# Optimization experiments

Measured on AMD Instinct MI355X. Metric: run time of the kernel, lower is better.

## Reference

```python
import jax, jax.numpy as jnp
import numpy as np

B, N, P = 16, 128, 4096          # images, proposals/img, pairs/img
D_IN, D_HID = 1024, 512          # input_dim, hidden_dim
D_GEO, D_EMB = 128, 200          # geometry_feat_dim, embed_dim
N_OBJ, N_REL = 151, 51           # obj classes, rel classes (out_dim = 50)
OUT = N_REL - 1
LN_EPS = 1e-5


def _ln(x, g, b):
    mu = jnp.mean(x, axis=-1, keepdims=True)
    var = jnp.var(x, axis=-1, keepdims=True)
    return (x - mu) * jax.lax.rsqrt(var + LN_EPS) * g + b


def setup_inputs() -> dict:
    key = jax.random.key(0)
    ks = jax.random.split(key, 20)
    w = lambda k, shape: (jax.random.normal(k, shape, jnp.float32) * 0.02)
    return {
        'visual_feat': jax.random.normal(ks[0], (B * P, D_IN), jnp.float32),
        'box_info': jax.random.uniform(ks[1], (B, N, 9), jnp.float32),
        'pred_logits': jax.random.normal(ks[2], (B, N, N_OBJ), jnp.float32),
        'pair_idx': jax.random.randint(ks[3], (B, P, 2), 0, N, jnp.int32),
        'obj_sem_w': w(ks[4], (N_OBJ, D_EMB)),
        'pos_w1': w(ks[5], (9, D_GEO)), 'pos_b1': jnp.zeros((D_GEO,), jnp.float32),
        'pos_w2': w(ks[6], (D_GEO, D_GEO)), 'pos_b2': jnp.zeros((D_GEO,), jnp.float32),
        'vis_w': w(ks[7], (D_IN, D_HID)), 'vis_b': jnp.zeros((D_HID,), jnp.float32),
        'geo_w': w(ks[8], (2 * D_EMB + 2 * D_GEO, D_HID)), 'geo_b': jnp.zeros((D_HID,), jnp.float32),
        'fus_g': jnp.ones((2 * D_HID,), jnp.float32), 'fus_bt': jnp.zeros((2 * D_HID,), jnp.float32),
        'fus_w': w(ks[9], (2 * D_HID, D_HID)), 'fus_b': jnp.zeros((D_HID,), jnp.float32),
        'cls_g': jnp.ones((D_HID,), jnp.float32), 'cls_bt': jnp.zeros((D_HID,), jnp.float32),
        'cls_w': w(ks[10], (D_HID, OUT)), 'cls_b': jnp.zeros((OUT,), jnp.float32),
    }


def reference(visual_feat, box_info, pred_logits, pair_idx,
              obj_sem_w, pos_w1, pos_b1, pos_w2, pos_b2,
              vis_w, vis_b, geo_w, geo_b,
              fus_g, fus_bt, fus_w, fus_b,
              cls_g, cls_bt, cls_w, cls_b):
    # detach() in torch -> stop_gradient
    vf = jax.lax.stop_gradient(visual_feat)
    pl = jax.lax.stop_gradient(pred_logits)
    # vis_embed = Sequential(ReLU, Linear): [B*P, D_IN] -> [B, P, D_HID]
    vis = (jnp.maximum(vf, 0.0) @ vis_w + vis_b).reshape(B, P, D_HID)
    # obj_pos_embed = Linear, ReLU, Linear: [B, N, 9] -> [B, N, D_GEO]
    pos = jnp.maximum(box_info @ pos_w1 + pos_b1, 0.0) @ pos_w2 + pos_b2
    # semantic embed: softmax over obj classes @ embedding table -> [B, N, D_EMB]
    sem = jax.nn.softmax(pl, axis=-1) @ obj_sem_w
    bidx = jnp.arange(B)[:, None]
    s, o = pair_idx[..., 0], pair_idx[..., 1]
    # gather pair reps: [B, P, 2*(D_GEO+D_EMB)]
    rep = jnp.concatenate([pos[bidx, s], sem[bidx, s], pos[bidx, o], sem[bidx, o]], axis=-1)
    # proposal_box_feat_extract = Sequential(ReLU, Linear)
    geo = jnp.maximum(rep, 0.0) @ geo_w + geo_b
    # proposal_feat_fusion = Sequential(LayerNorm, ReLU, Linear)
    fused = jnp.concatenate([vis, geo], axis=-1)
    fused = jnp.maximum(_ln(fused, fus_g, fus_bt), 0.0) @ fus_w + fus_b
    # proposal_relness_cls_fc = Sequential(LayerNorm, ReLU, Linear)
    logits = jnp.maximum(_ln(fused, cls_g, cls_bt), 0.0) @ cls_w + cls_b  # [B, P, OUT]
    # predictor_type == 'single': scatter max sigmoid score into NxN matrix
    scores = jnp.max(jax.nn.sigmoid(logits), axis=-1)  # [B, P]
    rel_mat = jnp.zeros((B, N, N), logits.dtype).at[bidx, s, o].set(scores)
    return logits.reshape(B * P, OUT), rel_mat
```

## Files before the change

kernel.cpp:

```cpp
#include <hip/hip_runtime.h>
#include <cstdint>

#define B_    16
#define N_    128
#define P_    4096
#define M_    65536
#define DIN   1024
#define DHID  512
#define DGEO  128
#define DEMB  200
#define NODEF 328
#define NOBJ  151
#define OUTC  50
#define KGEO  656
#define KGEOP 672

typedef __attribute__((ext_vector_type(8))) short bf16x8;
typedef __attribute__((ext_vector_type(4))) float f32x4;

typedef __attribute__((address_space(3))) unsigned char lds_u8;
typedef __attribute__((address_space(1))) unsigned char glb_u8;

static __device__ __forceinline__ void async_copy16(const void* g, void* l) {
  __builtin_amdgcn_global_load_lds((const glb_u8*)g, (lds_u8*)l, 16, 0, 0);
}

static __device__ __forceinline__ unsigned short f2b(float f) {
  union { float f; unsigned u; } v; v.f = f;
  unsigned r = v.u + 0x7fffu + ((v.u >> 16) & 1u);
  return (unsigned short)(r >> 16);
}
static __device__ __forceinline__ float b2f(unsigned short b) {
  union { unsigned u; float f; } v; v.u = ((unsigned)b) << 16;
  return v.f;
}
static __device__ __forceinline__ unsigned pack2(float a, float b) {
  return (unsigned)f2b(a) | ((unsigned)f2b(b) << 16);
}
static __device__ __forceinline__ void unpack8(uint4 raw, float* x) {
  x[0] = b2f(raw.x & 0xffffu); x[1] = b2f(raw.x >> 16);
  x[2] = b2f(raw.y & 0xffffu); x[3] = b2f(raw.y >> 16);
  x[4] = b2f(raw.z & 0xffffu); x[5] = b2f(raw.z >> 16);
  x[6] = b2f(raw.w & 0xffffu); x[7] = b2f(raw.w >> 16);
}

#define ZN   131072
#define TV   (512 * 1024)
#define TG   (512 * KGEOP)
#define TF   (512 * 1024)
#define TC   (128 * 512)
#define PREP_TOT (ZN + TV + TG + TF + TC)
__global__ __launch_bounds__(256)
void prep_kernel(uint4* __restrict__ scat,
                 const float* __restrict__ vis_w, unsigned short* __restrict__ wT_vis,
                 const float* __restrict__ geo_w, unsigned short* __restrict__ wT_geo,
                 const float* __restrict__ fus_w, unsigned short* __restrict__ wT_fus,
                 const float* __restrict__ cls_w, unsigned short* __restrict__ wT_cls) {
  int idx = blockIdx.x * 256 + threadIdx.x;
  if (idx < ZN) { scat[idx] = make_uint4(0, 0, 0, 0); return; }
  idx -= ZN;
  if (idx < TV) {
    int n = idx >> 10, k = idx & 1023;
    wT_vis[idx] = f2b(vis_w[(size_t)k * 512 + n]);
    return;
  }
  idx -= TV;
  if (idx < TG) {
    int n = idx / KGEOP, k = idx - n * KGEOP;
    wT_geo[idx] = (k < KGEO) ? f2b(geo_w[(size_t)k * 512 + n]) : 0;
    return;
  }
  idx -= TG;
  if (idx < TF) {
    int n = idx >> 10, k = idx & 1023;
    wT_fus[idx] = f2b(fus_w[(size_t)k * 512 + n]);
    return;
  }
  idx -= TF;
  if (idx < TC) {
    int n = idx >> 9, k = idx & 511;
    wT_cls[idx] = (n < OUTC) ? f2b(cls_w[(size_t)k * OUTC + n]) : 0;
  }
}

__global__ __launch_bounds__(128)
void node_kernel(const float* __restrict__ box, const float* __restrict__ plog,
                 const float* __restrict__ semw,
                 const float* __restrict__ w1, const float* __restrict__ b1,
                 const float* __restrict__ w2, const float* __restrict__ b2,
                 unsigned short* __restrict__ nodeFb) {
  const int node = blockIdx.x;
  const int t = threadIdx.x;
  __shared__ float sBox[9];
  __shared__ float sH[128];
  __shared__ float sE[NOBJ];
  __shared__ float sRed[4];
  if (t < 9) sBox[t] = box[node * 9 + t];
  float l0 = (t < NOBJ) ? plog[node * NOBJ + t] : -1e30f;
  float l1 = (t + 128 < NOBJ) ? plog[node * NOBJ + t + 128] : -1e30f;
  __syncthreads();
  float h = b1[t];
#pragma unroll
  for (int i = 0; i < 9; i++) h = fmaf(sBox[i], w1[i * 128 + t], h);
  h = fmaxf(h, 0.f);
  sH[t] = h;
  float mx = fmaxf(l0, l1);
#pragma unroll
  for (int off = 32; off >= 1; off >>= 1) mx = fmaxf(mx, __shfl_xor(mx, off));
  if ((t & 63) == 0) sRed[t >> 6] = mx;
  __syncthreads();
  mx = fmaxf(sRed[0], sRed[1]);
  float e0 = (t < NOBJ) ? expf(l0 - mx) : 0.f;
  float e1 = (t + 128 < NOBJ) ? expf(l1 - mx) : 0.f;
  if (t < NOBJ) sE[t] = e0;
  if (t + 128 < NOBJ) sE[t + 128] = e1;
  float sm = e0 + e1;
#pragma unroll
  for (int off = 32; off >= 1; off >>= 1) sm += __shfl_xor(sm, off);
  if ((t & 63) == 0) sRed[2 + (t >> 6)] = sm;
  __syncthreads();
  const float inv = 1.f / (sRed[2] + sRed[3]);
  float pv = b2[t];
  for (int i = 0; i < 128; i++) pv = fmaf(sH[i], w2[i * 128 + t], pv);
  nodeFb[(size_t)node * NODEF + t] = f2b(fmaxf(pv, 0.f));
  float a0 = 0.f, a1 = 0.f;
  const int d1 = (t + 128 < DEMB) ? (t + 128) : 0;
  for (int i = 0; i < NOBJ; i++) {
    float e = sE[i];
    a0 = fmaf(e, semw[i * DEMB + t], a0);
    a1 = fmaf(e, semw[i * DEMB + d1], a1);
  }
  nodeFb[(size_t)node * NODEF + 128 + t] = f2b(fmaxf(a0 * inv, 0.f));
  if (t + 128 < DEMB) nodeFb[(size_t)node * NODEF + 128 + t + 128] = f2b(fmaxf(a1 * inv, 0.f));
}

template<int D>
__global__ __launch_bounds__(256)
void ln_relu_kernel(unsigned short* __restrict__ X,
                    const float* __restrict__ g, const float* __restrict__ bta) {
  constexpr int C = D / 64;
  const int lane = threadIdx.x & 63, wv = threadIdx.x >> 6;
  const size_t row = (size_t)blockIdx.x * 4 + wv;
  unsigned short* xp = X + row * D + lane * C;
  float x[C];
#pragma unroll
  for (int c = 0; c < C; c += 8) {
    uint4 raw = *(const uint4*)(xp + c);
    unpack8(raw, x + c);
  }
  float s = 0.f, s2 = 0.f;
#pragma unroll
  for (int q = 0; q < C; q++) { s += x[q]; s2 = fmaf(x[q], x[q], s2); }
#pragma unroll
  for (int off = 32; off >= 1; off >>= 1) { s += __shfl_xor(s, off); s2 += __shfl_xor(s2, off); }
  const float mu = s / D;
  const float rs = rsqrtf(s2 / D - mu * mu + 1e-5f);
  const float* gp = g + lane * C;
  const float* bp = bta + lane * C;
#pragma unroll
  for (int c = 0; c < C; c += 8) {
    float4 g0 = *(const float4*)(gp + c), g1 = *(const float4*)(gp + c + 4);
    float4 t0 = *(const float4*)(bp + c), t1 = *(const float4*)(bp + c + 4);
    float y0 = fmaxf(fmaf((x[c + 0] - mu) * rs, g0.x, t0.x), 0.f);
    float y1 = fmaxf(fmaf((x[c + 1] - mu) * rs, g0.y, t0.y), 0.f);
    float y2 = fmaxf(fmaf((x[c + 2] - mu) * rs, g0.z, t0.z), 0.f);
    float y3 = fmaxf(fmaf((x[c + 3] - mu) * rs, g0.w, t0.w), 0.f);
    float y4 = fmaxf(fmaf((x[c + 4] - mu) * rs, g1.x, t1.x), 0.f);
    float y5 = fmaxf(fmaf((x[c + 5] - mu) * rs, g1.y, t1.y), 0.f);
    float y6 = fmaxf(fmaf((x[c + 6] - mu) * rs, g1.z, t1.z), 0.f);
    float y7 = fmaxf(fmaf((x[c + 7] - mu) * rs, g1.w, t1.w), 0.f);
    uint4 u;
    u.x = pack2(y0, y1); u.y = pack2(y2, y3);
    u.z = pack2(y4, y5); u.w = pack2(y6, y7);
    *(uint4*)(xp + c) = u;
  }
}

static __device__ __forceinline__ int pair_swz(int bid, int nwg) {
  const int cpx2 = nwg >> 4;
  const int pr = bid >> 1, q = bid & 1;
  return (((pr & 7) * cpx2) + (pr >> 3)) * 2 + q;
}

template<int MODE>
__global__ __launch_bounds__(512)
void gemm256r(const unsigned short* __restrict__ A, int ldaE,
              const unsigned short* __restrict__ Bt, int ldbE,
              const float* __restrict__ bias,
              unsigned short* __restrict__ C, int ldcE, int ccol0,
              int NS, int NBN,
              const int* __restrict__ pidx,
              const unsigned short* __restrict__ nodeFb,
              const unsigned short* __restrict__ zsrc) {
  __shared__ __align__(16) unsigned char smem[131072];
  const int tid = threadIdx.x;
  const int lane = tid & 63, w = tid >> 6;
  const int swz = pair_swz(blockIdx.x, gridDim.x);
  const int bm = swz / NBN, bn = swz - bm * NBN;

  const int sslot = (tid & 3) ^ ((tid >> 3) & 3);
  const int srow = tid >> 2;
  const size_t ldaBy = (size_t)ldaE * 2, ldbBy = (size_t)ldbE * 2;
  const unsigned char* aG = (const unsigned char*)A + (size_t)(bm * 256 + srow) * ldaBy + sslot * 16;
  const unsigned char* bG = (const unsigned char*)Bt + (size_t)(bn * 256 + srow) * ldbBy + sslot * 16;

  const unsigned short* nbS[2];
  const unsigned short* nbO[2];
  if (MODE == 1) {
#pragma unroll
    for (int r = 0; r < 2; r++) {
      int pr = bm * 256 + r * 128 + srow;
      int2 so = *(const int2*)(pidx + 2 * pr);
      int b = pr >> 12;
      nbS[r] = nodeFb + (size_t)((b << 7) + so.x) * NODEF;
      nbO[r] = nodeFb + (size_t)((b << 7) + so.y) * NODEF;
    }
  }

  auto stage = [&](int s) {
    const int slot = s & 3;
    unsigned char* la = smem + slot * 16384 + w * 1024;
    unsigned char* lb = smem + 65536 + slot * 16384 + w * 1024;
    if (MODE == 0) {
      const unsigned char* sa = aG + (size_t)s * 64;
      async_copy16(sa, la);
      async_copy16(sa + 128 * ldaBy, la + 8192);
    } else {
      const int e = s * 32 + sslot * 8;
#pragma unroll
      for (int r = 0; r < 2; r++) {
        uintptr_t ps = (uintptr_t)(nbS[r] + e);
        uintptr_t po = (uintptr_t)(nbO[r] + (e - NODEF));
        uintptr_t pz = (uintptr_t)zsrc;
        uintptr_t sel = (e < NODEF) ? ps : ((e < KGEO) ? po : pz);
        async_copy16((const void*)sel, la + r * 8192);
      }
    }
    const unsigned char* sb = bG + (size_t)s * 64;
    async_copy16(sb, lb);
    async_copy16(sb + 128 * ldbBy, lb + 8192);
  };

  const int wm = w >> 2, wn = w & 3;
  const int frow = lane & 15;
  const int colb = (((lane >> 4) ^ ((frow >> 1) & 3)) << 4);
  const int aRowB = (wm * 128 + frow) * 64;
  const int bRowB = (wn * 64 + frow) * 64;

  f32x4 acc[8][4];
#pragma unroll
  for (int m = 0; m < 8; m++)
#pragma unroll
    for (int n = 0; n < 4; n++) acc[m][n] = (f32x4){0.f, 0.f, 0.f, 0.f};

  stage(0); stage(1); stage(2);
  for (int s = 0; s < NS; ++s) {
    if (s == NS - 1)      asm volatile("s_waitcnt vmcnt(0)" ::: "memory");
    else if (s == NS - 2) asm volatile("s_waitcnt vmcnt(4)" ::: "memory");
    else                  asm volatile("s_waitcnt vmcnt(8)" ::: "memory");
    __builtin_amdgcn_s_barrier();
    __builtin_amdgcn_sched_barrier(0);
    if (s + 3 < NS) stage(s + 3);
    const unsigned char* ab = smem + (s & 3) * 16384;
    const unsigned char* bb = smem + 65536 + (s & 3) * 16384;
    bf16x8 af[8], bfv[4];
#pragma unroll
    for (int m = 0; m < 8; m++) af[m] = *(const bf16x8*)(ab + aRowB + m * 1024 + colb);
#pragma unroll
    for (int n = 0; n < 4; n++) bfv[n] = *(const bf16x8*)(bb + bRowB + n * 1024 + colb);
    __builtin_amdgcn_s_setprio(1);
#pragma unroll
    for (int m = 0; m < 8; m++)
#pragma unroll
      for (int n = 0; n < 4; n++)
        acc[m][n] = __builtin_amdgcn_mfma_f32_16x16x32_bf16(af[m], bfv[n], acc[m][n], 0, 0, 0);
    __builtin_amdgcn_s_setprio(0);
    __builtin_amdgcn_sched_barrier(0);
  }
  const int rb = bm * 256 + wm * 128 + ((lane >> 4) << 2);
  const int cb = bn * 256 + wn * 64 + frow;
#pragma unroll
  for (int n = 0; n < 4; n++) {
    const int col = cb + n * 16;
    const float bv = bias[col];
#pragma unroll
    for (int m = 0; m < 8; m++)
#pragma unroll
      for (int i = 0; i < 4; i++) {
        const int row = rb + m * 16 + i;
        C[(size_t)row * ldcE + ccol0 + col] = f2b(acc[m][n][i] + bv);
      }
  }
}

__global__ __launch_bounds__(512)
void gemm256f(const float* __restrict__ A,
              const unsigned short* __restrict__ Bt,
              const float* __restrict__ bias,
              unsigned short* __restrict__ C, int ldcE, int ccol0,
              int NBN) {
  constexpr int NS = 32;
  __shared__ __align__(16) unsigned char smem[131072];
  const int tid = threadIdx.x;
  const int lane = tid & 63, w = tid >> 6;
  const int swz = pair_swz(blockIdx.x, gridDim.x);
  const int bm = swz / NBN, bn = swz - bm * NBN;

  const int sslot = (tid & 3) ^ ((tid >> 3) & 3);
  const int srow = tid >> 2;
  const float* aG = A + (size_t)(bm * 256 + srow) * 1024 + sslot * 8;
  const unsigned char* bG = (const unsigned char*)Bt + (size_t)(bn * 256 + srow) * 2048 + sslot * 16;
  unsigned char* laBase = smem + (srow * 64) + (tid & 3) * 16;
  unsigned char* lbBase = smem + 65536 + w * 1024;

  uint4 ra0[4], ra1[4];

  auto issueA = [&](int s, uint4* ra) {
    const float* p0 = aG + (size_t)s * 32;
    ra[0] = *(const uint4*)(p0);
    ra[1] = *(const uint4*)(p0 + 4);
    ra[2] = *(const uint4*)(p0 + 128 * 1024);
    ra[3] = *(const uint4*)(p0 + 128 * 1024 + 4);
  };
  auto issueB = [&](int s) {
    const int slot = s & 3;
    const unsigned char* sb = bG + (size_t)s * 64;
    async_copy16(sb, lbBase + slot * 16384);
    async_copy16(sb + 128 * 2048, lbBase + slot * 16384 + 8192);
  };
  auto writeA = [&](int s, const uint4* ra) {
    const int slot = s & 3;
#pragma unroll
    for (int r = 0; r < 2; r++) {
      float x0 = fmaxf(__uint_as_float(ra[2 * r].x), 0.f);
      float x1 = fmaxf(__uint_as_float(ra[2 * r].y), 0.f);
      float x2 = fmaxf(__uint_as_float(ra[2 * r].z), 0.f);
      float x3 = fmaxf(__uint_as_float(ra[2 * r].w), 0.f);
      float x4 = fmaxf(__uint_as_float(ra[2 * r + 1].x), 0.f);
      float x5 = fmaxf(__uint_as_float(ra[2 * r + 1].y), 0.f);
      float x6 = fmaxf(__uint_as_float(ra[2 * r + 1].z), 0.f);
      float x7 = fmaxf(__uint_as_float(ra[2 * r + 1].w), 0.f);
      uint4 u;
      u.x = pack2(x0, x1); u.y = pack2(x2, x3);
      u.z = pack2(x4, x5); u.w = pack2(x6, x7);
      *(uint4*)(laBase + slot * 16384 + r * 8192) = u;
    }
  };

  const int wm = w >> 2, wn = w & 3;
  const int frow = lane & 15;
  const int colb = (((lane >> 4) ^ ((frow >> 1) & 3)) << 4);
  const int aRowB = (wm * 128 + frow) * 64;
  const int bRowB = (wn * 64 + frow) * 64;

  f32x4 acc[8][4];
#pragma unroll
  for (int m = 0; m < 8; m++)
#pragma unroll
    for (int n = 0; n < 4; n++) acc[m][n] = (f32x4){0.f, 0.f, 0.f, 0.f};

  issueA(0, ra0); issueB(0);
  issueA(1, ra1); issueB(1);

#pragma unroll 1
  for (int s = 0; s < NS; s += 2) {
#pragma unroll
    for (int half = 0; half < 2; half++) {
      const int sc = s + half;
      uint4* raC = half ? ra1 : ra0;
      if (sc == NS - 1) asm volatile("s_waitcnt vmcnt(0)" ::: "memory");
      else              asm volatile("s_waitcnt vmcnt(6)" ::: "memory");
      __builtin_amdgcn_sched_barrier(0);
      writeA(sc, raC);
      if (sc + 2 < NS) { issueA(sc + 2, raC); issueB(sc + 2); }
      asm volatile("s_waitcnt lgkmcnt(0)" ::: "memory");
      __builtin_amdgcn_s_barrier();
      __builtin_amdgcn_sched_barrier(0);
      const unsigned char* ab = smem + (sc & 3) * 16384;
      const unsigned char* bb = smem + 65536 + (sc & 3) * 16384;
      bf16x8 af[8], bfv[4];
#pragma unroll
      for (int m = 0; m < 8; m++) af[m] = *(const bf16x8*)(ab + aRowB + m * 1024 + colb);
#pragma unroll
      for (int n = 0; n < 4; n++) bfv[n] = *(const bf16x8*)(bb + bRowB + n * 1024 + colb);
      __builtin_amdgcn_s_setprio(1);
#pragma unroll
      for (int m = 0; m < 8; m++)
#pragma unroll
        for (int n = 0; n < 4; n++)
          acc[m][n] = __builtin_amdgcn_mfma_f32_16x16x32_bf16(af[m], bfv[n], acc[m][n], 0, 0, 0);
      __builtin_amdgcn_s_setprio(0);
      __builtin_amdgcn_sched_barrier(0);
      __builtin_amdgcn_s_barrier();
    }
  }
  const int rb = bm * 256 + wm * 128 + ((lane >> 4) << 2);
  const int cb = bn * 256 + wn * 64 + frow;
#pragma unroll
  for (int n = 0; n < 4; n++) {
    const int col = cb + n * 16;
    const float bv = bias[col];
#pragma unroll
    for (int m = 0; m < 8; m++)
#pragma unroll
      for (int i = 0; i < 4; i++) {
        const int row = rb + m * 16 + i;
        C[(size_t)row * ldcE + ccol0 + col] = f2b(acc[m][n][i] + bv);
      }
  }
}

__global__ __launch_bounds__(256)
void gemm_cls(const unsigned short* __restrict__ A, int lda,
              const unsigned short* __restrict__ Bt,
              const float* __restrict__ bias,
              float* __restrict__ C,
              int Ktot,
              const int* __restrict__ pidx,
              unsigned long long* __restrict__ scat) {
  __shared__ unsigned short ldsA[128 * 64];
  __shared__ unsigned short ldsB[128 * 64];
  const int tid = threadIdx.x;
  const int lane = tid & 63, wid = tid >> 6;
  const int cpx = gridDim.x >> 3;
  const int bm = (blockIdx.x & 7) * cpx + (blockIdx.x >> 3);

  const int srow = wid * 32 + (lane >> 3);
  const int skof = (lane & 7) * 8;
  const unsigned short* ag = A + (size_t)(bm * 128 + srow) * lda + skof;
  const unsigned short* bg = Bt + (size_t)srow * Ktot + skof;

  f32x4 acc[4][4];
#pragma unroll
  for (int m = 0; m < 4; m++)
#pragma unroll
    for (int n = 0; n < 4; n++) acc[m][n] = (f32x4){0.f, 0.f, 0.f, 0.f};

  const int wm = wid >> 1, wn = wid & 1;
  const int frow = lane & 15;
  const int kgrp = (lane >> 4) << 3;

  for (int kt = 0; kt < Ktot; kt += 64) {
#pragma unroll
    for (int i = 0; i < 4; i++) {
      async_copy16(ag + (size_t)i * 8 * lda + kt, &ldsA[wid * 2048 + i * 512]);
      async_copy16(bg + (size_t)i * 8 * Ktot + kt, &ldsB[wid * 2048 + i * 512]);
    }
    __syncthreads();
#pragma unroll
    for (int kk = 0; kk < 64; kk += 32) {
      bf16x8 af[4], bfr[4];
#pragma unroll
      for (int m = 0; m < 4; m++)
        af[m] = *(const bf16x8*)&ldsA[(wm * 64 + m * 16 + frow) * 64 + kk + kgrp];
#pragma unroll
      for (int n = 0; n < 4; n++)
        bfr[n] = *(const bf16x8*)&ldsB[(wn * 64 + n * 16 + frow) * 64 + kk + kgrp];
#pragma unroll
      for (int m = 0; m < 4; m++)
#pragma unroll
        for (int n = 0; n < 4; n++)
          acc[m][n] = __builtin_amdgcn_mfma_f32_16x16x32_bf16(af[m], bfr[n], acc[m][n], 0, 0, 0);
    }
    __syncthreads();
  }
  const int rb = bm * 128 + wm * 64 + ((lane >> 4) << 2);
#pragma unroll
  for (int n = 0; n < 4; n++) {
    const int col = wn * 64 + frow + n * 16;
    const float bv = (col < OUTC) ? bias[col] : 0.f;
#pragma unroll
    for (int m = 0; m < 4; m++)
#pragma unroll
      for (int i = 0; i < 4; i++) {
        const int row = rb + m * 16 + i;
        if (col < OUTC) C[(size_t)row * OUTC + col] = acc[m][n][i] + bv;
      }
  }
  if (wn == 0) {
#pragma unroll
    for (int m = 0; m < 4; m++)
#pragma unroll
      for (int i = 0; i < 4; i++) {
        float mx = -1e30f;
#pragma unroll
        for (int n = 0; n < 4; n++) {
          const int col = n * 16 + frow;
          float v = acc[m][n][i] + ((col < OUTC) ? bias[col] : 0.f);
          if (col < OUTC) mx = fmaxf(mx, v);
        }
        mx = fmaxf(mx, __shfl_xor(mx, 1));
        mx = fmaxf(mx, __shfl_xor(mx, 2));
        mx = fmaxf(mx, __shfl_xor(mx, 4));
        mx = fmaxf(mx, __shfl_xor(mx, 8));
        if (frow == 0) {
          const int row = rb + m * 16 + i;
          float sc = 1.f / (1.f + expf(-mx));
          int b = row >> 12, p = row & 4095;
          int s = pidx[2 * row], o = pidx[2 * row + 1];
          unsigned long long key = (((unsigned long long)(p + 1)) << 32) |
                                   (unsigned long long)__float_as_uint(sc);
          atomicMax(&scat[((size_t)(b * N_ + s) << 7) + o], key);
        }
      }
  }
}

__global__ void relmat_kernel(const unsigned long long* __restrict__ scat, float* __restrict__ out) {
  int i = blockIdx.x * blockDim.x + threadIdx.x;
  if (i >= B_ * N_ * N_) return;
  unsigned long long v = scat[i];
  out[i] = v ? __uint_as_float((unsigned)(v & 0xffffffffu)) : 0.f;
}

extern "C" void kernel_launch(void* const* d_in, const int* in_sizes, int n_in,
                              void* d_out, int out_size, void* d_ws, size_t ws_size,
                              hipStream_t stream) {
  const float* visual_feat = (const float*)d_in[0];
  const float* box_info    = (const float*)d_in[1];
  const float* pred_logits = (const float*)d_in[2];
  const int*   pair_idx    = (const int*)d_in[3];
  const float* obj_sem_w   = (const float*)d_in[4];
  const float* pos_w1 = (const float*)d_in[5];
  const float* pos_b1 = (const float*)d_in[6];
  const float* pos_w2 = (const float*)d_in[7];
  const float* pos_b2 = (const float*)d_in[8];
  const float* vis_w  = (const float*)d_in[9];
  const float* vis_b  = (const float*)d_in[10];
  const float* geo_w  = (const float*)d_in[11];
  const float* geo_b  = (const float*)d_in[12];
  const float* fus_g  = (const float*)d_in[13];
  const float* fus_bt = (const float*)d_in[14];
  const float* fus_w  = (const float*)d_in[15];
  const float* fus_b  = (const float*)d_in[16];
  const float* cls_g  = (const float*)d_in[17];
  const float* cls_bt = (const float*)d_in[18];
  const float* cls_w  = (const float*)d_in[19];
  const float* cls_b  = (const float*)d_in[20];

  char* ws = (char*)d_ws;
  size_t off = 0;
  auto alloc = [&](size_t bytes) { char* p = ws + off; off += (bytes + 255) & ~(size_t)255; return p; };
  unsigned short* fused = (unsigned short*)alloc((size_t)M_ * 1024 * 2);
  unsigned short* fused2 = (unsigned short*)alloc((size_t)M_ * 512 * 2);
  unsigned short* nodeFb = (unsigned short*)alloc((size_t)B_ * N_ * NODEF * 2);
  unsigned short* wT_vis = (unsigned short*)alloc((size_t)512 * 1024 * 2);
  unsigned short* wT_geo = (unsigned short*)alloc((size_t)512 * KGEOP * 2);
  unsigned short* wT_fus = (unsigned short*)alloc((size_t)512 * 1024 * 2);
  unsigned short* wT_cls = (unsigned short*)alloc((size_t)128 * 512 * 2);
  unsigned long long* scat = (unsigned long long*)alloc((size_t)B_ * N_ * N_ * 8);

  float* out_logits = (float*)d_out;
  float* out_rel = out_logits + (size_t)M_ * OUTC;

  prep_kernel<<<dim3((PREP_TOT + 255) / 256), 256, 0, stream>>>(
      (uint4*)scat, vis_w, wT_vis, geo_w, wT_geo, fus_w, wT_fus, cls_w, wT_cls);
  node_kernel<<<dim3(B_ * N_), 128, 0, stream>>>(box_info, pred_logits, obj_sem_w,
                                                 pos_w1, pos_b1, pos_w2, pos_b2, nodeFb);
  gemm256r<1><<<dim3(512), 512, 0, stream>>>(nullptr, 0, wT_geo, KGEOP, geo_b,
                                             fused, 1024, 512, KGEOP / 32, 2,
                                             pair_idx, nodeFb, (const unsigned short*)scat);
  gemm256f<<<dim3(512), 512, 0, stream>>>(visual_feat, wT_vis, vis_b,
                                          fused, 1024, 0, 2);
  ln_relu_kernel<1024><<<dim3(M_ / 4), 256, 0, stream>>>(fused, fus_g, fus_bt);
  gemm256r<0><<<dim3(512), 512, 0, stream>>>(fused, 1024, wT_fus, 1024, fus_b,
                                             fused2, 512, 0, 1024 / 32, 2,
                                             nullptr, nullptr, nullptr);
  ln_relu_kernel<512><<<dim3(M_ / 4), 256, 0, stream>>>(fused2, cls_g, cls_bt);
  gemm_cls<<<dim3(512), 256, 0, stream>>>(fused2, 512, wT_cls, cls_b,
                                          out_logits, 512, pair_idx, scat);
  relmat_kernel<<<dim3((B_ * N_ * N_) / 256), 256, 0, stream>>>(scat, out_rel);
}
```

Before: 443.4 us.

## Shrink visual GEMM tile to 128x256 with double buffering for higher occupancy

The fp32-input visual projection GEMM moves from a 256x256 tile with a 4-stage LDS ring (128 KB) to a 128x256 tile with a 2-stage ring (48 KB) and a launch-bounds hint for several blocks per CU, doubling the grid. B fragments are now loaded inside the MFMA loop, and the B async copy is issued after the trailing barrier. The aim is more resident waves to hide the fp32 A-load latency, at the cost of less reuse per B tile (B is reloaded twice as often) and shallower prefetch.

```diff
diff --git a/kernel.cpp b/kernel.cpp
--- a/kernel.cpp
+++ b/kernel.cpp
@@ -293,14 +293,14 @@
   }
 }
 
-__global__ __launch_bounds__(512)
-void gemm256f(const float* __restrict__ A,
-              const unsigned short* __restrict__ Bt,
-              const float* __restrict__ bias,
-              unsigned short* __restrict__ C, int ldcE, int ccol0,
-              int NBN) {
+__global__ __launch_bounds__(512, 4)
+void gemm256f3(const float* __restrict__ A,
+               const unsigned short* __restrict__ Bt,
+               const float* __restrict__ bias,
+               unsigned short* __restrict__ C, int ldcE, int ccol0,
+               int NBN) {
   constexpr int NS = 32;
-  __shared__ __align__(16) unsigned char smem[131072];
+  __shared__ __align__(16) unsigned char smem[49152];
   const int tid = threadIdx.x;
   const int lane = tid & 63, w = tid >> 6;
   const int swz = pair_swz(blockIdx.x, gridDim.x);
@@ -308,54 +308,49 @@
 
   const int sslot = (tid & 3) ^ ((tid >> 3) & 3);
   const int srow = tid >> 2;
-  const float* aG = A + (size_t)(bm * 256 + srow) * 1024 + sslot * 8;
+  const float* aG = A + (size_t)(bm * 128 + srow) * 1024 + sslot * 8;
   const unsigned char* bG = (const unsigned char*)Bt + (size_t)(bn * 256 + srow) * 2048 + sslot * 16;
-  unsigned char* laBase = smem + (srow * 64) + (tid & 3) * 16;
-  unsigned char* lbBase = smem + 65536 + w * 1024;
-
-  uint4 ra0[4], ra1[4];
+  unsigned char* laBase = smem + srow * 64 + (tid & 3) * 16;
+  unsigned char* lbBase = smem + 16384 + w * 1024;
+
+  uint4 ra0[2], ra1[2];
 
   auto issueA = [&](int s, uint4* ra) {
     const float* p0 = aG + (size_t)s * 32;
     ra[0] = *(const uint4*)(p0);
     ra[1] = *(const uint4*)(p0 + 4);
-    ra[2] = *(const uint4*)(p0 + 128 * 1024);
-    ra[3] = *(const uint4*)(p0 + 128 * 1024 + 4);
   };
   auto issueB = [&](int s) {
-    const int slot = s & 3;
+    const int slot = s & 1;
     const unsigned char* sb = bG + (size_t)s * 64;
     async_copy16(sb, lbBase + slot * 16384);
     async_copy16(sb + 128 * 2048, lbBase + slot * 16384 + 8192);
   };
   auto writeA = [&](int s, const uint4* ra) {
-    const int slot = s & 3;
-#pragma unroll
-    for (int r = 0; r < 2; r++) {
-      float x0 = fmaxf(__uint_as_float(ra[2 * r].x), 0.f);
-      float x1 = fmaxf(__uint_as_float(ra[2 * r].y), 0.f);
-      float x2 = fmaxf(__uint_as_float(ra[2 * r].z), 0.f);
-      float x3 = fmaxf(__uint_as_float(ra[2 * r].w), 0.f);
-      float x4 = fmaxf(__uint_as_float(ra[2 * r + 1].x), 0.f);
-      float x5 = fmaxf(__uint_as_float(ra[2 * r + 1].y), 0.f);
-      float x6 = fmaxf(__uint_as_float(ra[2 * r + 1].z), 0.f);
-      float x7 = fmaxf(__uint_as_float(ra[2 * r + 1].w), 0.f);
-      uint4 u;
-      u.x = pack2(x0, x1); u.y = pack2(x2, x3);
-      u.z = pack2(x4, x5); u.w = pack2(x6, x7);
-      *(uint4*)(laBase + slot * 16384 + r * 8192) = u;
-    }
+    const int slot = s & 1;
+    float x0 = fmaxf(__uint_as_float(ra[0].x), 0.f);
+    float x1 = fmaxf(__uint_as_float(ra[0].y), 0.f);
+    float x2 = fmaxf(__uint_as_float(ra[0].z), 0.f);
+    float x3 = fmaxf(__uint_as_float(ra[0].w), 0.f);
+    float x4 = fmaxf(__uint_as_float(ra[1].x), 0.f);
+    float x5 = fmaxf(__uint_as_float(ra[1].y), 0.f);
+    float x6 = fmaxf(__uint_as_float(ra[1].z), 0.f);
+    float x7 = fmaxf(__uint_as_float(ra[1].w), 0.f);
+    uint4 u;
+    u.x = pack2(x0, x1); u.y = pack2(x2, x3);
+    u.z = pack2(x4, x5); u.w = pack2(x6, x7);
+    *(uint4*)(laBase + slot * 8192) = u;
   };
 
   const int wm = w >> 2, wn = w & 3;
   const int frow = lane & 15;
   const int colb = (((lane >> 4) ^ ((frow >> 1) & 3)) << 4);
-  const int aRowB = (wm * 128 + frow) * 64;
+  const int aRowB = (wm * 64 + frow) * 64;
   const int bRowB = (wn * 64 + frow) * 64;
 
-  f32x4 acc[8][4];
-#pragma unroll
-  for (int m = 0; m < 8; m++)
+  f32x4 acc[4][4];
+#pragma unroll
+  for (int m = 0; m < 4; m++)
 #pragma unroll
     for (int n = 0; n < 4; n++) acc[m][n] = (f32x4){0.f, 0.f, 0.f, 0.f};
 
@@ -369,39 +364,41 @@
       const int sc = s + half;
       uint4* raC = half ? ra1 : ra0;
       if (sc == NS - 1) asm volatile("s_waitcnt vmcnt(0)" ::: "memory");
-      else              asm volatile("s_waitcnt vmcnt(6)" ::: "memory");
+      else              asm volatile("s_waitcnt vmcnt(4)" ::: "memory");
       __builtin_amdgcn_sched_barrier(0);
       writeA(sc, raC);
-      if (sc + 2 < NS) { issueA(sc + 2, raC); issueB(sc + 2); }
+      if (sc + 2 < NS) issueA(sc + 2, raC);
       asm volatile("s_waitcnt lgkmcnt(0)" ::: "memory");
       __builtin_amdgcn_s_barrier();
       __builtin_amdgcn_sched_barrier(0);
-      const unsigned char* ab = smem + (sc & 3) * 16384;
-      const unsigned char* bb = smem + 65536 + (sc & 3) * 16384;
-      bf16x8 af[8], bfv[4];
-#pragma unroll
-      for (int m = 0; m < 8; m++) af[m] = *(const bf16x8*)(ab + aRowB + m * 1024 + colb);
-#pragma unroll
-      for (int n = 0; n < 4; n++) bfv[n] = *(const bf16x8*)(bb + bRowB + n * 1024 + colb);
+      const unsigned char* ab = smem + (sc & 1) * 8192;
+      const unsigned char* bb = smem + 16384 + (sc & 1) * 16384;
+      bf16x8 af[4];
+#pragma unroll
+      for (int m = 0; m < 4; m++) af[m] = *(const bf16x8*)(ab + aRowB + m * 1024 + colb);
       __builtin_amdgcn_s_setprio(1);
 #pragma unroll
-      for (int m = 0; m < 8; m++)
-#pragma unroll
-        for (int n = 0; n < 4; n++)
-          acc[m][n] = __builtin_amdgcn_mfma_f32_16x16x32_bf16(af[m], bfv[n], acc[m][n], 0, 0, 0);
+      for (int n = 0; n < 4; n++) {
+        bf16x8 bf = *(const bf16x8*)(bb + bRowB + n * 1024 + colb);
+#pragma unroll
+        for (int m = 0; m < 4; m++)
+          acc[m][n] = __builtin_amdgcn_mfma_f32_16x16x32_bf16(af[m], bf, acc[m][n], 0, 0, 0);
+      }
       __builtin_amdgcn_s_setprio(0);
       __builtin_amdgcn_sched_barrier(0);
       __builtin_amdgcn_s_barrier();
+      __builtin_amdgcn_sched_barrier(0);
+      if (sc + 2 < NS) issueB(sc + 2);
     }
   }
-  const int rb = bm * 256 + wm * 128 + ((lane >> 4) << 2);
+  const int rb = bm * 128 + wm * 64 + ((lane >> 4) << 2);
   const int cb = bn * 256 + wn * 64 + frow;
 #pragma unroll
   for (int n = 0; n < 4; n++) {
     const int col = cb + n * 16;
     const float bv = bias[col];
 #pragma unroll
-    for (int m = 0; m < 8; m++)
+    for (int m = 0; m < 4; m++)
 #pragma unroll
       for (int i = 0; i < 4; i++) {
         const int row = rb + m * 16 + i;
@@ -560,8 +557,8 @@
   gemm256r<1><<<dim3(512), 512, 0, stream>>>(nullptr, 0, wT_geo, KGEOP, geo_b,
                                              fused, 1024, 512, KGEOP / 32, 2,
                                              pair_idx, nodeFb, (const unsigned short*)scat);
-  gemm256f<<<dim3(512), 512, 0, stream>>>(visual_feat, wT_vis, vis_b,
-                                          fused, 1024, 0, 2);
+  gemm256f3<<<dim3(1024), 512, 0, stream>>>(visual_feat, wT_vis, vis_b,
+                                            fused, 1024, 0, 2);
   ln_relu_kernel<1024><<<dim3(M_ / 4), 256, 0, stream>>>(fused, fus_g, fus_bt);
   gemm256r<0><<<dim3(512), 512, 0, stream>>>(fused, 1024, wT_fus, 1024, fus_b,
                                              fused2, 512, 0, 1024 / 32, 2,
```

After: 429.6 us. 1.03x faster.
